# Kernel optimization log

Measured on AMD Instinct MI355X. Metric: run time of the kernel, lower is better.

The kernel has to match this reference:

```python
import jax, jax.numpy as jnp
import numpy as np

B, D, C, L, H = 4096, 768, 512, 32, 256
E = C * L  # total flattened extension embeddings

def _l2norm(x, eps=1e-12):
    n = jnp.sqrt(jnp.sum(x * x, axis=-1, keepdims=True))
    return x / jnp.maximum(n, eps)

def setup_inputs() -> dict:
    key = jax.random.key(0)
    ks = jax.random.split(key, 8)
    text_feat = jax.random.normal(ks[0], (B, D), dtype=jnp.float32)
    img_feat = jax.random.normal(ks[1], (B, D), dtype=jnp.float32)
    ext_embs = _l2norm(jax.random.normal(ks[2], (E, D), dtype=jnp.float32))
    concept_names = _l2norm(jax.random.normal(ks[3], (C, D), dtype=jnp.float32))
    # each concept has exactly L extension embeddings; sorted segment ids
    segment_ids = jnp.repeat(jnp.arange(C, dtype=jnp.int32), L)
    W1 = jax.random.normal(ks[4], (C + D, H), dtype=jnp.float32) * (1.0 / np.sqrt(C + D))
    b1 = jnp.zeros((H,), dtype=jnp.float32)
    W2 = jax.random.normal(ks[5], (H, C), dtype=jnp.float32) * (1.0 / np.sqrt(H))
    b2 = jnp.zeros((C,), dtype=jnp.float32)
    alpha = jnp.float32(0.5)
    temperature = jnp.float32(0.07)
    return {"text_feat": text_feat, "img_feat": img_feat, "ext_embs": ext_embs,
            "segment_ids": segment_ids, "concept_names": concept_names,
            "W1": W1, "b1": b1, "W2": W2, "b2": b2,
            "alpha": alpha, "temperature": temperature}

def reference(text_feat, img_feat, ext_embs, segment_ids, concept_names,
              W1, b1, W2, b2, alpha, temperature):
    # query = normalize(text + img)
    q = _l2norm(text_feat + img_feat)                      # [B, D]
    # ragged per-concept max similarity: one big GEMM + segmented max
    sim = jnp.einsum('bd,ed->be', q, ext_embs)            # [B, E]
    prior = jax.ops.segment_max(sim.T, segment_ids,
                                num_segments=C,
                                indices_are_sorted=True).T  # [B, C]
    # small MLP -> temperature softmax -> weighted concept sum
    h = jax.nn.relu(jnp.concatenate([prior, q], axis=-1) @ W1 + b1)  # [B, H]
    logits = h @ W2 + b2                                   # [B, C]
    weights = jax.nn.softmax(logits / temperature, axis=-1)
    dyn_prompt = weights @ concept_names                   # [B, D]
    combined = text_feat + alpha * dyn_prompt
    return _l2norm(combined)
```

## Files before the change

### kernel.cpp

```cpp
#include <hip/hip_runtime.h>
#include <hip/hip_bf16.h>

typedef unsigned short bfu;
typedef __attribute__((ext_vector_type(4))) float f32x4;
typedef __attribute__((ext_vector_type(8))) short bf16x8;
typedef __attribute__((ext_vector_type(4))) int i32x4;
typedef __attribute__((ext_vector_type(8))) int i32x8;

__device__ __forceinline__ unsigned short f2bf(float f) {
    unsigned int u = __float_as_uint(f);
    u += 0x7FFFu + ((u >> 16) & 1u);
    return (unsigned short)(u >> 16);
}

__device__ __forceinline__ unsigned pack_fp8x4(float a, float b, float c, float d) {
    int u = __builtin_amdgcn_cvt_pk_fp8_f32(a, b, 0, false);
    u = __builtin_amdgcn_cvt_pk_fp8_f32(c, d, u, true);
    return (unsigned)u;
}

__device__ __forceinline__ void gload_lds16(const void* g, void* l) {
    __builtin_amdgcn_global_load_lds(
        (const __attribute__((address_space(1))) unsigned int*)g,
        (__attribute__((address_space(3))) unsigned int*)l, 16, 0, 0);
}

__device__ __forceinline__ float block_sum256(float v, float* sm) {
    #pragma unroll
    for (int off = 32; off; off >>= 1) v += __shfl_xor(v, off);
    int w = threadIdx.x >> 6;
    if ((threadIdx.x & 63) == 0) sm[w] = v;
    __syncthreads();
    float r = sm[0] + sm[1] + sm[2] + sm[3];
    __syncthreads();
    return r;
}

__device__ __forceinline__ float block_max256(float v, float* sm) {
    #pragma unroll
    for (int off = 32; off; off >>= 1) v = fmaxf(v, __shfl_xor(v, off));
    int w = threadIdx.x >> 6;
    if ((threadIdx.x & 63) == 0) sm[w] = v;
    __syncthreads();
    float r = fmaxf(fmaxf(sm[0], sm[1]), fmaxf(sm[2], sm[3]));
    __syncthreads();
    return r;
}

__global__ __launch_bounds__(256) void prep_kernel(const float* __restrict__ text,
                                                   const float* __restrict__ img,
                                                   bfu* __restrict__ X,
                                                   unsigned* __restrict__ Q8,
                                                   const float* __restrict__ ext,
                                                   unsigned* __restrict__ E8,
                                                   const float* __restrict__ W1, bfu* __restrict__ W1t,
                                                   const float* __restrict__ W2, bfu* __restrict__ W2t,
                                                   const float* __restrict__ cn, bfu* __restrict__ cnt) {
    __shared__ float sm[4];
    int b = blockIdx.x, t = threadIdx.x;
    if (b < 4096) {
        int row = b;
        float4 v = {0.f, 0.f, 0.f, 0.f};
        if (t < 192) {
            float4 a = ((const float4*)(text + (size_t)row * 768))[t];
            float4 c = ((const float4*)(img + (size_t)row * 768))[t];
            v.x = a.x + c.x; v.y = a.y + c.y; v.z = a.z + c.z; v.w = a.w + c.w;
        }
        float ss = v.x * v.x + v.y * v.y + v.z * v.z + v.w * v.w;
        float tot = block_sum256(ss, sm);
        float inv = 1.0f / fmaxf(sqrtf(tot), 1e-12f);
        if (t < 192) {
            ushort4 o = make_ushort4(f2bf(v.x * inv), f2bf(v.y * inv), f2bf(v.z * inv), f2bf(v.w * inv));
            ((ushort4*)(X + (size_t)row * 1280 + 512))[t] = o;
            float s16 = inv * 16.0f;
            Q8[(size_t)row * 192 + t] = pack_fp8x4(v.x * s16, v.y * s16, v.z * s16, v.w * s16);
        }
    } else if (b < 16384) {
        int i = (b - 4096) * 256 + t;
        float4 v = ((const float4*)ext)[i];
        E8[i] = pack_fp8x4(v.x * 16.0f, v.y * 16.0f, v.z * 16.0f, v.w * 16.0f);
    } else if (b < 17664) {
        int idx = (b - 16384) * 256 + t;
        int c = idx / 1280, r = idx - c * 1280;
        W1t[idx] = f2bf(W1[(size_t)r * 256 + c]);
    } else if (b < 18176) {
        int idx = (b - 17664) * 256 + t;
        int c = idx / 256, r = idx - c * 256;
        W2t[idx] = f2bf(W2[(size_t)r * 512 + c]);
    } else {
        int idx = (b - 18176) * 256 + t;
        int c = idx / 512, r = idx - c * 512;
        cnt[idx] = f2bf(cn[(size_t)r * 768 + c]);
    }
}

__device__ __forceinline__ i32x8 ld_frag256(const char* s, int row, int lq, int ks) {
    const int r7 = row & 7;
    const int base = row * 256 + (ks << 7);
    i32x4 lo = *(const i32x4*)(s + base + ((((lq << 1))     ^ r7) << 4));
    i32x4 hi = *(const i32x4*)(s + base + ((((lq << 1) | 1) ^ r7) << 4));
    i32x8 v;
    v[0] = lo[0]; v[1] = lo[1]; v[2] = lo[2]; v[3] = lo[3];
    v[4] = hi[0]; v[5] = hi[1]; v[6] = hi[2]; v[7] = hi[3];
    return v;
}

__global__ __launch_bounds__(512) void sim_segmax_kernel(const unsigned char* __restrict__ Q8,
                                                         const unsigned char* __restrict__ E8,
                                                         bfu* __restrict__ X) {
    __shared__ __align__(16) char sA[2][128 * 256];
    __shared__ __align__(16) char sB[2][128 * 256];
    const int bm = blockIdx.x & 31;
    const int bn = blockIdx.x >> 5;
    const int m0 = bm << 7, n0 = bn << 7;
    const int t = threadIdx.x, lane = t & 63, wv = t >> 6;
    const int wm = (wv >> 2) << 6;
    const int wn = (wv & 3) << 5;
    const int lr = lane & 15, lq = lane >> 4;

    f32x4 zero = {0.f, 0.f, 0.f, 0.f};
    f32x4 acc[4][2];
    #pragma unroll
    for (int i = 0; i < 4; ++i)
        #pragma unroll
        for (int j = 0; j < 2; ++j) acc[i][j] = zero;

    auto stage = [&](int slot, int k0) {
        int row = t >> 4, c = t & 15;
        int cs = c ^ (row & 7);
        const unsigned char* gA = Q8 + (size_t)(m0 + row) * 768 + k0 + (cs << 4);
        const unsigned char* gB = E8 + (size_t)(n0 + row) * 768 + k0 + (cs << 4);
        char* lA = sA[slot] + (wv << 10);
        char* lB = sB[slot] + (wv << 10);
        #pragma unroll
        for (int i = 0; i < 4; ++i) {
            gload_lds16(gA, lA);
            gA += 32 * 768; lA += 512 * 16;
        }
        #pragma unroll
        for (int i = 0; i < 4; ++i) {
            gload_lds16(gB, lB);
            gB += 32 * 768; lB += 512 * 16;
        }
    };

    stage(0, 0);
    stage(1, 256);
    __builtin_amdgcn_sched_barrier(0);
    asm volatile("s_waitcnt vmcnt(8)" ::: "memory");
    __builtin_amdgcn_sched_barrier(0);
    __builtin_amdgcn_s_barrier();
    __builtin_amdgcn_sched_barrier(0);

    #pragma unroll
    for (int kk = 0; kk < 3; ++kk) {
        if (kk == 1) stage(0, 512);
        const char* bufA = sA[kk & 1];
        const char* bufB = sB[kk & 1];
        #pragma unroll
        for (int ks = 0; ks < 2; ++ks) {
            i32x8 af[4], bf[2];
            #pragma unroll
            for (int f = 0; f < 4; ++f)
                af[f] = ld_frag256(bufA, wm + f * 16 + lr, lq, ks);
            #pragma unroll
            for (int j = 0; j < 2; ++j)
                bf[j] = ld_frag256(bufB, wn + j * 16 + lr, lq, ks);
            #pragma unroll
            for (int i = 0; i < 4; ++i)
                #pragma unroll
                for (int j = 0; j < 2; ++j)
                    acc[i][j] = __builtin_amdgcn_mfma_scale_f32_16x16x128_f8f6f4(
                        af[i], bf[j], acc[i][j], 0, 0, 0, 0x7F7F7F7F, 0, 0x7F7F7F7F);
        }
        if (kk < 2) {
            __builtin_amdgcn_sched_barrier(0);
            asm volatile("s_waitcnt vmcnt(0)" ::: "memory");
            asm volatile("s_waitcnt lgkmcnt(0)" ::: "memory");
            __builtin_amdgcn_sched_barrier(0);
            __builtin_amdgcn_s_barrier();
            __builtin_amdgcn_sched_barrier(0);
        }
    }

    const float sc = 0.00390625f;
    const int g = (n0 + wn) >> 5;
    #pragma unroll
    for (int i = 0; i < 4; ++i) {
        #pragma unroll
        for (int r = 0; r < 4; ++r) {
            float v = fmaxf(acc[i][0][r], acc[i][1][r]);
            #pragma unroll
            for (int off = 8; off; off >>= 1)
                v = fmaxf(v, __shfl_xor(v, off));
            if (lr == 0) {
                int row = m0 + wm + i * 16 + lq * 4 + r;
                X[(size_t)row * 1280 + g] = f2bf(v * sc);
            }
        }
    }
}

template <int BM>
__device__ __forceinline__ void gemm_mainloop(const bfu* A, const bfu* B, int K,
                                              int lda, int ldb, int m0, int n0,
                                              short* sA, short* sB, f32x4 acc[BM / 32][4]) {
    const int t = threadIdx.x, lane = t & 63, wv = t >> 6;
    const int wm = (wv >> 1) * (BM / 2), wn = (wv & 1) << 6;
    const int lr = lane & 15, lq = lane >> 4;

    i32x4 ra[BM / 32], rb[4];
    auto ldg = [&](int k0) {
        #pragma unroll
        for (int i = 0; i < BM / 32; ++i) {
            int idx = i * 256 + t;
            int row = idx >> 3, cg = idx & 7;
            ra[i] = *(const i32x4*)(A + (size_t)(m0 + row) * lda + k0 + (cg << 3));
        }
        #pragma unroll
        for (int i = 0; i < 4; ++i) {
            int idx = i * 256 + t;
            int row = idx >> 3, cg = idx & 7;
            rb[i] = *(const i32x4*)(B + (size_t)(n0 + row) * ldb + k0 + (cg << 3));
        }
    };
    auto st_lds = [&]() {
        #pragma unroll
        for (int i = 0; i < BM / 32; ++i) {
            int idx = i * 256 + t;
            int row = idx >> 3, cg = idx & 7, cs = cg ^ (row & 7);
            *(i32x4*)(sA + row * 64 + cs * 8) = ra[i];
        }
        #pragma unroll
        for (int i = 0; i < 4; ++i) {
            int idx = i * 256 + t;
            int row = idx >> 3, cg = idx & 7, cs = cg ^ (row & 7);
            *(i32x4*)(sB + row * 64 + cs * 8) = rb[i];
        }
    };

    const int NIT = K >> 6;
    ldg(0);
    for (int kk = 0; kk < NIT; ++kk) {
        if (kk) __syncthreads();
        st_lds();
        __syncthreads();
        if (kk + 1 < NIT) ldg((kk + 1) * 64);
        #pragma unroll
        for (int ks = 0; ks < 2; ++ks) {
            bf16x8 af[BM / 32], bfr[4];
            #pragma unroll
            for (int f = 0; f < BM / 32; ++f) {
                int mrow = wm + f * 16 + lr;
                int c = ks * 4 + lq;
                af[f] = *(const bf16x8*)(sA + mrow * 64 + ((c ^ (mrow & 7)) << 3));
            }
            #pragma unroll
            for (int f = 0; f < 4; ++f) {
                int nrow = wn + f * 16 + lr;
                int c = ks * 4 + lq;
                bfr[f] = *(const bf16x8*)(sB + nrow * 64 + ((c ^ (nrow & 7)) << 3));
            }
            #pragma unroll
            for (int i = 0; i < BM / 32; ++i)
                #pragma unroll
                for (int j = 0; j < 4; ++j)
                    acc[i][j] = __builtin_amdgcn_mfma_f32_16x16x32_bf16(af[i], bfr[j], acc[i][j], 0, 0, 0);
        }
    }
}

template <int EPI, int BM>
__global__ __launch_bounds__(256) void gemm_kernel(const bfu* __restrict__ A,
                                                   const bfu* __restrict__ B,
                                                   const float* __restrict__ bias,
                                                   void* __restrict__ out,
                                                   int K, int lda, int ldb, int N, int ntN) {
    __shared__ __align__(16) short sA[BM * 64];
    __shared__ __align__(16) short sB[128 * 64];
    int bm = blockIdx.x / ntN, bn = blockIdx.x - bm * ntN;
    int m0 = bm * BM, n0 = bn * 128;
    f32x4 zero = {0.f, 0.f, 0.f, 0.f};
    f32x4 acc[BM / 32][4];
    #pragma unroll
    for (int i = 0; i < BM / 32; ++i)
        #pragma unroll
        for (int j = 0; j < 4; ++j) acc[i][j] = zero;

    gemm_mainloop<BM>(A, B, K, lda, ldb, m0, n0, sA, sB, acc);

    const int t = threadIdx.x, lane = t & 63, wv = t >> 6;
    const int wm = (wv >> 1) * (BM / 2), wn = (wv & 1) << 6;
    const int lr = lane & 15, lq = lane >> 4;
    #pragma unroll
    for (int j = 0; j < 4; ++j) {
        int col = n0 + wn + j * 16 + lr;
        float bv = (EPI >= 1) ? bias[col] : 0.0f;
        #pragma unroll
        for (int i = 0; i < BM / 32; ++i) {
            #pragma unroll
            for (int r = 0; r < 4; ++r) {
                int row = m0 + wm + i * 16 + lq * 4 + r;
                float v = acc[i][j][r] + bv;
                if (EPI == 1) {
                    v = fmaxf(v, 0.0f);
                    ((bfu*)out)[(size_t)row * N + col] = f2bf(v);
                } else {
                    ((float*)out)[(size_t)row * N + col] = v;
                }
            }
        }
    }
}

__global__ __launch_bounds__(256) void softmax_kernel(const float* __restrict__ logits,
                                                      const float* __restrict__ temp,
                                                      bfu* __restrict__ wout) {
    __shared__ float sm[4];
    int row = blockIdx.x, t = threadIdx.x;
    float invT = 1.0f / temp[0];
    float l0 = logits[(size_t)row * 512 + t];
    float l1 = logits[(size_t)row * 512 + 256 + t];
    float m = block_max256(fmaxf(l0, l1), sm);
    float e0 = __expf((l0 - m) * invT);
    float e1 = __expf((l1 - m) * invT);
    float s = block_sum256(e0 + e1, sm);
    float inv = 1.0f / s;
    wout[(size_t)row * 512 + t]       = f2bf(e0 * inv);
    wout[(size_t)row * 512 + 256 + t] = f2bf(e1 * inv);
}

__global__ __launch_bounds__(256) void final_kernel(const float* __restrict__ text,
                                                    const float* __restrict__ dyn,
                                                    const float* __restrict__ alpha,
                                                    float* __restrict__ out) {
    __shared__ float sm[4];
    int row = blockIdx.x, t = threadIdx.x;
    float a = alpha[0];
    float v[3]; float ss = 0.f;
    #pragma unroll
    for (int i = 0; i < 3; ++i) {
        size_t o = (size_t)row * 768 + t + 256 * i;
        v[i] = text[o] + a * dyn[o];
        ss += v[i] * v[i];
    }
    float tot = block_sum256(ss, sm);
    float inv = 1.0f / fmaxf(sqrtf(tot), 1e-12f);
    #pragma unroll
    for (int i = 0; i < 3; ++i)
        out[(size_t)row * 768 + t + 256 * i] = v[i] * inv;
}

extern "C" void kernel_launch(void* const* d_in, const int* in_sizes, int n_in,
                              void* d_out, int out_size, void* d_ws, size_t ws_size,
                              hipStream_t stream) {
    const float* text  = (const float*)d_in[0];
    const float* img   = (const float*)d_in[1];
    const float* ext   = (const float*)d_in[2];
    const float* cn    = (const float*)d_in[4];
    const float* W1    = (const float*)d_in[5];
    const float* b1    = (const float*)d_in[6];
    const float* W2    = (const float*)d_in[7];
    const float* b2    = (const float*)d_in[8];
    const float* alpha = (const float*)d_in[9];
    const float* temp  = (const float*)d_in[10];
    float* out = (float*)d_out;

    char* p = (char*)d_ws;
    auto carve = [&](size_t bytes) -> char* {
        char* r = p; p += (bytes + 255) & ~(size_t)255; return r;
    };
    unsigned char* E8 = (unsigned char*)carve((size_t)16384 * 768);
    unsigned char* Q8 = (unsigned char*)carve((size_t)4096 * 768);
    bfu*   X      = (bfu*)carve((size_t)4096 * 1280 * 2);
    bfu*   W1t    = (bfu*)carve((size_t)256 * 1280 * 2);
    bfu*   W2t    = (bfu*)carve((size_t)512 * 256 * 2);
    bfu*   cnt    = (bfu*)carve((size_t)768 * 512 * 2);
    bfu*   Hm     = (bfu*)carve((size_t)4096 * 256 * 2);
    float* logits = (float*)carve((size_t)4096 * 512 * 4);
    bfu*   wts    = (bfu*)carve((size_t)4096 * 512 * 2);
    float* dyn    = (float*)carve((size_t)4096 * 768 * 4);

    prep_kernel<<<19712, 256, 0, stream>>>(text, img, X, (unsigned*)Q8,
                                           ext, (unsigned*)E8, W1, W1t, W2, W2t, cn, cnt);
    sim_segmax_kernel<<<4096, 512, 0, stream>>>(Q8, E8, X);
    gemm_kernel<1, 64><<<64 * 2, 256, 0, stream>>>(X, W1t, b1, (void*)Hm, 1280, 1280, 1280, 256, 2);
    gemm_kernel<2, 64><<<64 * 4, 256, 0, stream>>>(Hm, W2t, b2, (void*)logits, 256, 256, 256, 512, 4);
    softmax_kernel<<<4096, 256, 0, stream>>>(logits, temp, wts);
    gemm_kernel<0, 64><<<64 * 6, 256, 0, stream>>>(wts, cnt, nullptr, (void*)dyn, 512, 512, 512, 768, 6);
    final_kernel<<<4096, 256, 0, stream>>>(text, dyn, alpha, out);
}
```

Baseline: 275.3 us.

## Fuse second MLP GEMM with temperature softmax in one kernel

Replaces the separate logits GEMM and row softmax kernels with one kernel that computes a 16-row by 512-column tile of H·W2 using MFMA. It then does the bias add, max, exp and sum reductions across the four waves in registers and shared memory. This removes the fp32 logits round trip through global memory and one kernel launch. In exchange only 256 blocks run, each reloading the full W2 slice per K step, which lowers parallelism and raises shared-memory use.

```diff
diff --git a/kernel.cpp b/kernel.cpp
--- a/kernel.cpp
+++ b/kernel.cpp
@@ -313,21 +313,114 @@
     }
 }
 
-__global__ __launch_bounds__(256) void softmax_kernel(const float* __restrict__ logits,
-                                                      const float* __restrict__ temp,
-                                                      bfu* __restrict__ wout) {
-    __shared__ float sm[4];
-    int row = blockIdx.x, t = threadIdx.x;
+__global__ __launch_bounds__(256) void gemm2_softmax_kernel(const bfu* __restrict__ A,
+                                                            const bfu* __restrict__ B,
+                                                            const float* __restrict__ bias,
+                                                            const float* __restrict__ temp,
+                                                            bfu* __restrict__ wout) {
+    __shared__ __align__(16) short sA[16 * 64];
+    __shared__ __align__(16) short sB[512 * 64];
+    __shared__ float smx[4][16], ssm[4][16];
+    const int m0 = blockIdx.x << 4;
+    const int t = threadIdx.x, lane = t & 63, wv = t >> 6;
+    const int wn = wv << 7;
+    const int lr = lane & 15, lq = lane >> 4;
+
+    f32x4 zero = {0.f, 0.f, 0.f, 0.f};
+    f32x4 acc[8];
+    #pragma unroll
+    for (int j = 0; j < 8; ++j) acc[j] = zero;
+
+    for (int kk = 0; kk < 4; ++kk) {
+        int k0 = kk * 64;
+        i32x4 ra;
+        if (t < 128) {
+            int row = t >> 3, cg = t & 7;
+            ra = *(const i32x4*)(A + (size_t)(m0 + row) * 256 + k0 + (cg << 3));
+        }
+        i32x4 rb[16];
+        #pragma unroll
+        for (int i = 0; i < 16; ++i) {
+            int idx = i * 256 + t;
+            int row = idx >> 3, cg = idx & 7;
+            rb[i] = *(const i32x4*)(B + (size_t)row * 256 + k0 + (cg << 3));
+        }
+        if (kk) __syncthreads();
+        if (t < 128) {
+            int row = t >> 3, cg = t & 7, cs = cg ^ (row & 7);
+            *(i32x4*)(sA + row * 64 + cs * 8) = ra;
+        }
+        #pragma unroll
+        for (int i = 0; i < 16; ++i) {
+            int idx = i * 256 + t;
+            int row = idx >> 3, cg = idx & 7, cs = cg ^ (row & 7);
+            *(i32x4*)(sB + row * 64 + cs * 8) = rb[i];
+        }
+        __syncthreads();
+        #pragma unroll
+        for (int ks = 0; ks < 2; ++ks) {
+            bf16x8 af, bfr[8];
+            {
+                int mrow = lr;
+                int c = ks * 4 + lq;
+                af = *(const bf16x8*)(sA + mrow * 64 + ((c ^ (mrow & 7)) << 3));
+            }
+            #pragma unroll
+            for (int f = 0; f < 8; ++f) {
+                int nrow = wn + f * 16 + lr;
+                int c = ks * 4 + lq;
+                bfr[f] = *(const bf16x8*)(sB + nrow * 64 + ((c ^ (nrow & 7)) << 3));
+            }
+            #pragma unroll
+            for (int j = 0; j < 8; ++j)
+                acc[j] = __builtin_amdgcn_mfma_f32_16x16x32_bf16(af, bfr[j], acc[j], 0, 0, 0);
+        }
+    }
+
     float invT = 1.0f / temp[0];
-    float l0 = logits[(size_t)row * 512 + t];
-    float l1 = logits[(size_t)row * 512 + 256 + t];
-    float m = block_max256(fmaxf(l0, l1), sm);
-    float e0 = __expf((l0 - m) * invT);
-    float e1 = __expf((l1 - m) * invT);
-    float s = block_sum256(e0 + e1, sm);
-    float inv = 1.0f / s;
-    wout[(size_t)row * 512 + t]       = f2bf(e0 * inv);
-    wout[(size_t)row * 512 + 256 + t] = f2bf(e1 * inv);
+    float bv[8];
+    #pragma unroll
+    for (int j = 0; j < 8; ++j) bv[j] = bias[wn + j * 16 + lr];
+
+    #pragma unroll
+    for (int rr = 0; rr < 4; ++rr) {
+        float m = -1e30f;
+        #pragma unroll
+        for (int j = 0; j < 8; ++j) m = fmaxf(m, acc[j][rr] + bv[j]);
+        #pragma unroll
+        for (int off = 8; off; off >>= 1) m = fmaxf(m, __shfl_xor(m, off));
+        if (lr == 0) smx[wv][lq * 4 + rr] = m;
+    }
+    __syncthreads();
+    float rm[4];
+    #pragma unroll
+    for (int rr = 0; rr < 4; ++rr) {
+        int idx = lq * 4 + rr;
+        rm[rr] = fmaxf(fmaxf(smx[0][idx], smx[1][idx]), fmaxf(smx[2][idx], smx[3][idx]));
+    }
+    #pragma unroll
+    for (int rr = 0; rr < 4; ++rr) {
+        float s = 0.f;
+        #pragma unroll
+        for (int j = 0; j < 8; ++j) {
+            float e = __expf((acc[j][rr] + bv[j] - rm[rr]) * invT);
+            acc[j][rr] = e;
+            s += e;
+        }
+        #pragma unroll
+        for (int off = 8; off; off >>= 1) s += __shfl_xor(s, off);
+        if (lr == 0) ssm[wv][lq * 4 + rr] = s;
+    }
+    __syncthreads();
+    #pragma unroll
+    for (int rr = 0; rr < 4; ++rr) {
+        int idx = lq * 4 + rr;
+        float inv = 1.0f / (ssm[0][idx] + ssm[1][idx] + ssm[2][idx] + ssm[3][idx]);
+        int row = m0 + idx;
+        #pragma unroll
+        for (int j = 0; j < 8; ++j)
+            wout[(size_t)row * 512 + wn + j * 16 + lr] = f2bf(acc[j][rr] * inv);
+    }
 }
 
 __global__ __launch_bounds__(256) void final_kernel(const float* __restrict__ text,
@@ -380,13 +473,13 @@
     float* logits = (float*)carve((size_t)4096 * 512 * 4);
     bfu*   wts    = (bfu*)carve((size_t)4096 * 512 * 2);
     float* dyn    = (float*)carve((size_t)4096 * 768 * 4);
+    (void)logits;
 
     prep_kernel<<<19712, 256, 0, stream>>>(text, img, X, (unsigned*)Q8,
                                            ext, (unsigned*)E8, W1, W1t, W2, W2t, cn, cnt);
     sim_segmax_kernel<<<4096, 512, 0, stream>>>(Q8, E8, X);
     gemm_kernel<1, 64><<<64 * 2, 256, 0, stream>>>(X, W1t, b1, (void*)Hm, 1280, 1280, 1280, 256, 2);
-    gemm_kernel<2, 64><<<64 * 4, 256, 0, stream>>>(Hm, W2t, b2, (void*)logits, 256, 256, 256, 512, 4);
-    softmax_kernel<<<4096, 256, 0, stream>>>(logits, temp, wts);
+    gemm2_softmax_kernel<<<256, 256, 0, stream>>>(Hm, W2t, b2, temp, wts);
     gemm_kernel<0, 64><<<64 * 6, 256, 0, stream>>>(wts, cnt, nullptr, (void*)dyn, 512, 512, 512, 768, 6);
     final_kernel<<<4096, 256, 0, stream>>>(text, dyn, alpha, out);
 }
```

Result: no change. 276.4 us (+0.4%).
